# Kernel optimization log

Measured on AMD Instinct MI355X. Metric: run time of the kernel, lower is better.

Reference implementation:

```python
import jax, jax.numpy as jnp
import numpy as np

N_ATOM = 30000
N_PAIR = 1_000_000
N_TRI = 4_000_000
N_SF = 16
RC = 6.0

LAMBD = jnp.array([-1.0, 1.0] * 8, dtype=jnp.float32)
ZETA = jnp.array([1.0, 1.0, 2.0, 2.0, 4.0, 4.0, 8.0, 8.0] * 2, dtype=jnp.float32)
ETA = jnp.array([0.01, 0.014, 0.02, 0.028, 0.04, 0.056, 0.08, 0.11,
                 0.16, 0.22, 0.32, 0.45, 0.63, 0.72, 0.9, 1.0], dtype=jnp.float32)


def cutoff_f1(r):
    # PiNN 'f1' cutoff: 0.5*(cos(pi*r/rc)+1)
    return 0.5 * (jnp.cos(jnp.float32(np.pi) * r / RC) + 1.0)


def gaussian_basis(r, fc):
    # GaussianBasis with center=0, gamma=eta: fc * exp(-eta * r^2), shape [n, n_sf]
    return fc[:, None] * jnp.exp(-ETA[None, :] * (r[:, None] ** 2))


def setup_inputs() -> dict:
    key = jax.random.key(0)
    k1, k2, k3, k4, k5 = jax.random.split(key, 5)
    ind_2 = jax.random.randint(k1, (N_PAIR, 2), 0, N_ATOM, dtype=jnp.int32)
    ind_3 = jax.random.randint(k2, (N_TRI, 2), 0, N_PAIR, dtype=jnp.int32)
    dist = jax.random.uniform(k3, (N_PAIR,), jnp.float32, 0.5, RC)
    dirs = jax.random.normal(k4, (N_PAIR, 3), jnp.float32)
    dirs = dirs / jnp.linalg.norm(dirs, axis=1, keepdims=True)
    diff = dirs * dist[:, None]  # bond vectors consistent with dist
    elems = jax.random.randint(k5, (N_ATOM,), 0, 4, dtype=jnp.int32)
    fc = cutoff_f1(dist)
    return {"ind_2": ind_2, "ind_3": ind_3, "dist": dist, "diff": diff,
            "elems": elems, "fc": fc}


def reference(ind_2, ind_3, dist, diff, elems, fc):
    # i=j=k='ALL': species filter is identity; a_rind = arange(n_atom)
    ind_ij = ind_3[:, 0]
    ind_ik = ind_3[:, 1]
    i_rind = ind_2[ind_ij, 0]  # central atom index per triplet

    diff_ij = diff[ind_ij]  # [T,3]
    diff_ik = diff[ind_ik]
    diff_jk = diff_ik - diff_ij
    dist_jk = jnp.linalg.norm(diff_jk, axis=1)
    mask = dist_jk < RC  # TF filters triplets; we mask (jit-friendly)

    fc_jk = cutoff_f1(dist_jk)
    dist_ij = dist[ind_ij]
    dist_ik = dist[ind_ik]
    fc_ij = fc[ind_ij]
    fc_ik = fc[ind_ik]

    cos_ijk = jnp.einsum('id,id->i', diff_ij, diff_ik) / dist_ij / dist_ik
    base = jnp.maximum(1.0 + LAMBD[None, :] * cos_ijk[:, None], 0.0)
    sf = (2.0 ** (1.0 - ZETA[None, :]) * base ** ZETA[None, :]
          * gaussian_basis(dist_ij, fc_ij)
          * gaussian_basis(dist_ik, fc_ik)
          * gaussian_basis(dist_jk, fc_jk))
    sf = jnp.where(mask[:, None], sf, 0.0)

    # scatter_nd add into per-atom fingerprints
    fp = jnp.zeros((N_ATOM, N_SF), dtype=sf.dtype).at[i_rind].add(sf)

    # jacobian indices: central-atom rel index per participating pair
    vals = jnp.where(mask, i_rind, -1)
    seg = jnp.concatenate([ind_ij, ind_ik])
    pair_i = jax.ops.segment_max(jnp.concatenate([vals, vals]), seg,
                                 num_segments=N_PAIR)
    pair_i = jnp.maximum(pair_i, -1)  # empty segments -> -1 sentinel
    jacob_ind = jnp.stack([jnp.arange(N_PAIR, dtype=jnp.int32), pair_i], axis=1)
    return fp, jacob_ind
```

## Files before the change

kernel.cpp:

```cpp
#include <hip/hip_runtime.h>

#define N_ATOM 30000
#define N_PAIR 1000000
#define N_TRI  4000000
#define N_SF   16
#define FP_ELEMS (N_ATOM * N_SF)

#define ASH  5
#define APB  32
#define NCB  938
#define NSUB 8
#define NSEG (NCB * NSUB)
#define OVF_CNT_IDX NSEG
#define OVF_CAP 131072
#define TILE 4096
#define PER_TH 16
#define NTILES ((N_TRI + TILE - 1) / TILE)

#define OFF_CCNT  0ULL
#define OFF_IKMAX 65536ULL
#define OFF_AOFP  4065536ULL
#define OFF_FLAG  6065536ULL
#define OFF_OVF   7065536ULL
#define OFF_PACK  8114112ULL
#define OFF_CB    24114112ULL

__device__ __constant__ float c_eta[16] = {
    0.01f, 0.014f, 0.02f, 0.028f, 0.04f, 0.056f, 0.08f, 0.11f,
    0.16f, 0.22f, 0.32f, 0.45f, 0.63f, 0.72f, 0.9f, 1.0f};

__device__ __forceinline__ bool tri_math_pack(
    float4 A, float4 B, float A8[8], float& R2)
{
    float ax = A.x, ay = A.y, az = A.z, fcij = A.w;
    float bx = B.x, by = B.y, bz = B.z, fcik = B.w;
    float d2ij = fmaf(ax, ax, fmaf(ay, ay, az * az));
    float d2ik = fmaf(bx, bx, fmaf(by, by, bz * bz));
    float jx = bx - ax, jy = by - ay, jz = bz - az;
    float d2jk = fmaf(jx, jx, fmaf(jy, jy, jz * jz));
    if (!(d2jk < 36.0f)) return false;
    float dij = sqrtf(d2ij);
    float dik = sqrtf(d2ik);
    float djk = sqrtf(d2jk);
    const float PI_OVER_RC = 0.5235987755982988f;
    float fcjk = 0.5f * (__cosf(PI_OVER_RC * djk) + 1.0f);
    float dot = fmaf(ax, bx, fmaf(ay, by, az * bz));
    float cosv = dot / (dij * dik);
    R2 = d2ij + d2ik + d2jk;
    float FCt = fcij * fcik * fcjk;
    float bm = fmaxf(1.0f - cosv, 0.0f);
    float bp = fmaxf(1.0f + cosv, 0.0f);
    float bm2 = bm * bm, bp2 = bp * bp;
    float bm4 = bm2 * bm2, bp4 = bp2 * bp2;
    float bm8 = bm4 * bm4, bp8 = bp4 * bp4;
    A8[0] = FCt * bm;              A8[1] = FCt * bp;
    A8[2] = 0.5f * FCt * bm2;      A8[3] = 0.5f * FCt * bp2;
    A8[4] = 0.125f * FCt * bm4;    A8[5] = 0.125f * FCt * bp4;
    A8[6] = 0.0078125f * FCt * bm8; A8[7] = 0.0078125f * FCt * bp8;
    return true;
}


__global__ __launch_bounds__(256) void prep2(
    const int2* __restrict__ ind2, const float* __restrict__ diff,
    const float* __restrict__ fc,
    int* __restrict__ ccnt, int* __restrict__ ikmax,
    unsigned short* __restrict__ aofp, unsigned char* __restrict__ flag,
    float4* __restrict__ pack, float* __restrict__ out)
{
    int p = blockIdx.x * blockDim.x + threadIdx.x;
    if (p <= NSEG) ccnt[p] = 0;
    if (p < FP_ELEMS) out[p] = 0.0f;
    if (p >= N_PAIR) return;
    ikmax[p] = -1;
    flag[p] = 0;
    aofp[p] = (unsigned short)ind2[p].x;
    float4 r;
    r.x = diff[3 * p + 0];
    r.y = diff[3 * p + 1];
    r.z = diff[3 * p + 2];
    r.w = fc[p];
    pack[p] = r;
}

__global__ __launch_bounds__(256) void bin3(
    const int2* __restrict__ ind3, const unsigned short* __restrict__ aofp,
    int* __restrict__ ccnt, int2* __restrict__ cbucket,
    int2* __restrict__ ovf, int cap)
{
    __shared__ int lcnt[NCB];
    __shared__ int lbase[NCB];
    const int thr = threadIdx.x;
    const int sub = blockIdx.x & (NSUB - 1);
    const long long t0 = (long long)blockIdx.x * TILE;

    for (int i = thr; i < NCB; i += 256) lcnt[i] = 0;
    __syncthreads();

    int myatom[PER_TH];
    int myslot[PER_TH];
#pragma unroll
    for (int j = 0; j < PER_TH; ++j) {
        long long t = t0 + j * 256 + thr;
        int a = 0, s = -1;
        if (t < N_TRI) {
            int ij = ind3[t].x;
            a = aofp[ij];
            s = atomicAdd(&lcnt[a >> ASH], 1);
        }
        myatom[j] = a;
        myslot[j] = s;
    }
    __syncthreads();
    for (int c = thr; c < NCB; c += 256) {
        int n = lcnt[c];
        lbase[c] = n ? atomicAdd(&ccnt[c * NSUB + sub], n) : 0;
    }
    __syncthreads();
#pragma unroll
    for (int j = 0; j < PER_TH; ++j) {
        long long t = t0 + j * 256 + thr;
        if (t >= N_TRI) continue;
        int a = myatom[j];
        int c = a >> ASH;
        int slot = lbase[c] + myslot[j];
        int2 pr = ind3[t];
        if (slot < cap) {
            int2 e;
            e.x = pr.x | ((a & (APB - 1)) << 20);
            e.y = pr.y;
            cbucket[(size_t)(c * NSUB + sub) * cap + slot] = e;
        } else {
            int o = atomicAdd(&ccnt[OVF_CNT_IDX], 1);
            if (o < OVF_CAP) ovf[o] = pr;
        }
    }
}

__global__ __launch_bounds__(256) void reduce4(
    const int* __restrict__ ccnt, const int2* __restrict__ cbucket, int cap,
    const float4* __restrict__ pack,
    int* __restrict__ ikmax, unsigned char* __restrict__ flag,
    float* __restrict__ out)
{
    __shared__ float lacc[APB * 17];
    const int seg = blockIdx.x;
    const int b = seg >> 3;
    const int thr = threadIdx.x;
    for (int i = thr; i < APB * 17; i += 256) lacc[i] = 0.0f;
    __syncthreads();

    int n = ccnt[seg];
    n = min(n, cap);
    const int2* segp = cbucket + (size_t)seg * cap;
    for (int i = thr; i < n; i += 256) {
        int2 e = segp[i];
        int a5 = (e.x >> 20) & (APB - 1);
        int ij = e.x & 0xFFFFF;
        int ik = e.y;
        float4 A = pack[ij];
        float4 B = pack[ik];
        float A8[8], R2;
        if (!tri_math_pack(A, B, A8, R2)) continue;
        flag[ij] = 1;
        atomicMax(&ikmax[ik], (b << ASH) + a5);
#pragma unroll
        for (int s = 0; s < 16; ++s)
            atomicAdd(&lacc[a5 * 17 + s], A8[s & 7] * __expf(-c_eta[s] * R2));
    }
    __syncthreads();
    for (int t = thr; t < APB * N_SF; t += 256) {
        int atom = (b << ASH) + (t >> 4);
        float v = lacc[(t >> 4) * 17 + (t & 15)];
        if (atom < N_ATOM && v != 0.0f)
            unsafeAtomicAdd(out + (size_t)atom * N_SF + (t & 15), v);
    }
}

__global__ __launch_bounds__(256) void ovf3(
    const int* __restrict__ ccnt, const int2* __restrict__ ovf,
    const float4* __restrict__ pack, const unsigned short* __restrict__ aofp,
    int* __restrict__ ikmax, unsigned char* __restrict__ flag,
    float* __restrict__ out)
{
    int i = blockIdx.x * blockDim.x + threadIdx.x;
    int n = ccnt[OVF_CNT_IDX];
    if (n > OVF_CAP) n = OVF_CAP;
    if (i >= n) return;
    int2 pr = ovf[i];
    int ij = pr.x, ik = pr.y;
    float A8[8], R2;
    if (!tri_math_pack(pack[ij], pack[ik], A8, R2)) return;
    int atom = aofp[ij];
    flag[ij] = 1;
    atomicMax(&ikmax[ik], atom);
    float* base = out + (size_t)atom * N_SF;
#pragma unroll
    for (int s = 0; s < 16; ++s)
        unsafeAtomicAdd(base + s, A8[s & 7] * __expf(-c_eta[s] * R2));
}

__global__ __launch_bounds__(256) void fin3(
    const int* __restrict__ ikmax, const unsigned char* __restrict__ flag,
    const unsigned short* __restrict__ aofp, float* __restrict__ out)
{
    int p = blockIdx.x * blockDim.x + threadIdx.x;
    if (p >= N_PAIR) return;
    int v = ikmax[p];
    if (flag[p]) { int a = aofp[p]; v = v > a ? v : a; }
    float* jf = out + FP_ELEMS;
    jf[2 * p + 0] = (float)p;
    jf[2 * p + 1] = (float)v;
}


__global__ __launch_bounds__(256) void init_legacy(float* __restrict__ out) {
    int i = blockIdx.x * blockDim.x + threadIdx.x;
    if (i < FP_ELEMS) out[i] = 0.0f;
    if (i < N_PAIR) ((int*)out + FP_ELEMS)[2 * i + 1] = -1;
}

__global__ __launch_bounds__(256) void tri_legacy(
    const int* __restrict__ ind2, const int2* __restrict__ ind3,
    const float* __restrict__ dist, const float* __restrict__ diff,
    const float* __restrict__ fc, float* __restrict__ out) {
    int t = blockIdx.x * blockDim.x + threadIdx.x;
    if (t >= N_TRI) return;
    int2 pr = ind3[t];
    int ij = pr.x, ik = pr.y;
    float4 A, B;
    A.x = diff[3 * ij + 0]; A.y = diff[3 * ij + 1]; A.z = diff[3 * ij + 2]; A.w = fc[ij];
    B.x = diff[3 * ik + 0]; B.y = diff[3 * ik + 1]; B.z = diff[3 * ik + 2]; B.w = fc[ik];
    float A8[8], R2;
    if (!tri_math_pack(A, B, A8, R2)) return;
    int atom = ind2[2 * ij];
    int* jac = (int*)out + FP_ELEMS;
    atomicMax(&jac[2 * ij + 1], atom);
    atomicMax(&jac[2 * ik + 1], atom);
    float* base = out + (size_t)atom * N_SF;
#pragma unroll
    for (int s = 0; s < 16; ++s)
        unsafeAtomicAdd(base + s, A8[s & 7] * __expf(-c_eta[s] * R2));
}

__global__ __launch_bounds__(256) void fin_legacy(float* __restrict__ out) {
    int p = blockIdx.x * blockDim.x + threadIdx.x;
    if (p >= N_PAIR) return;
    int* jac = (int*)out + FP_ELEMS;
    int v = jac[2 * p + 1];
    float* jf = (float*)jac;
    jf[2 * p + 0] = (float)p;
    jf[2 * p + 1] = (float)v;
}


extern "C" void kernel_launch(void* const* d_in, const int* in_sizes, int n_in,
                              void* d_out, int out_size, void* d_ws, size_t ws_size,
                              hipStream_t stream) {
    const int2*  ind2 = (const int2*)d_in[0];
    const int2*  ind3 = (const int2*)d_in[1];
    const float* dist = (const float*)d_in[2];
    const float* diff = (const float*)d_in[3];
    const float* fc   = (const float*)d_in[5];
    float* out = (float*)d_out;

    const size_t seg_stride = (size_t)NSEG * sizeof(int2);
    const size_t need_min = OFF_CB + seg_stride * 608;

    if (ws_size >= need_min) {
        char* ws = (char*)d_ws;
        int* ccnt            = (int*)(ws + OFF_CCNT);
        int* ikmax           = (int*)(ws + OFF_IKMAX);
        unsigned short* aofp = (unsigned short*)(ws + OFF_AOFP);
        unsigned char* flag  = (unsigned char*)(ws + OFF_FLAG);
        int2* ovf            = (int2*)(ws + OFF_OVF);
        float4* pack         = (float4*)(ws + OFF_PACK);
        int2* cbucket        = (int2*)(ws + OFF_CB);
        int cap = (int)((ws_size - OFF_CB) / seg_stride);
        if (cap > 1024) cap = 1024;

        int pb = (N_PAIR + 255) / 256;
        prep2<<<pb, 256, 0, stream>>>(ind2, diff, fc, ccnt, ikmax, aofp, flag, pack, out);
        bin3<<<NTILES, 256, 0, stream>>>(ind3, aofp, ccnt, cbucket, ovf, cap);
        reduce4<<<NSEG, 256, 0, stream>>>(ccnt, cbucket, cap, pack, ikmax, flag, out);
        ovf3<<<OVF_CAP / 256, 256, 0, stream>>>(ccnt, ovf, pack, aofp, ikmax, flag, out);
        fin3<<<pb, 256, 0, stream>>>(ikmax, flag, aofp, out);
    } else {
        init_legacy<<<(N_PAIR + 255) / 256, 256, 0, stream>>>(out);
        tri_legacy<<<(N_PAIR * 4 + 255) / 256, 256, 0, stream>>>((const int*)d_in[0], ind3, dist, diff, fc, out);
        fin_legacy<<<(N_PAIR + 255) / 256, 256, 0, stream>>>(out);
    }
}
```

Before: 447.5 us.

## Rework binning tile size and reduce kernel to wave-per-segment with unrolled gathers

The binning kernel now uses 512-thread blocks over 8192-triplet tiles and packs each triplet's atom id and local slot into one register, cutting register use. The reduction kernel is restructured so that each 64-lane wave handles one sub-segment, two waves per block share a chunk's LDS accumulator, and bucket entries plus pair gathers are issued four at a time ahead of the math to expose more memory-level parallelism. Sharing LDS accumulators across two sub-segments halves the number of global flush atomics. The risk is higher register pressure from the unrolled gathers and fewer sub-buckets per bin, since larger tiles make each sub-bucket fill faster and push more triplets into the overflow path.

```diff
diff --git a/kernel.cpp b/kernel.cpp
--- a/kernel.cpp
+++ b/kernel.cpp
@@ -13,9 +13,10 @@
 #define NSEG (NCB * NSUB)
 #define OVF_CNT_IDX NSEG
 #define OVF_CAP 131072
-#define TILE 4096
+#define TILE 8192
 #define PER_TH 16
 #define NTILES ((N_TRI + TILE - 1) / TILE)
+#define RUNROLL 4
 
 #define OFF_CCNT  0ULL
 #define OFF_IKMAX 65536ULL
@@ -83,7 +84,7 @@
     pack[p] = r;
 }
 
-__global__ __launch_bounds__(256) void bin3(
+__global__ __launch_bounds__(512) void bin3(
     const int2* __restrict__ ind3, const unsigned short* __restrict__ aofp,
     int* __restrict__ ccnt, int2* __restrict__ cbucket,
     int2* __restrict__ ovf, int cap)
@@ -94,36 +95,36 @@
     const int sub = blockIdx.x & (NSUB - 1);
     const long long t0 = (long long)blockIdx.x * TILE;
 
-    for (int i = thr; i < NCB; i += 256) lcnt[i] = 0;
-    __syncthreads();
-
-    int myatom[PER_TH];
-    int myslot[PER_TH];
+    for (int i = thr; i < NCB; i += 512) lcnt[i] = 0;
+    __syncthreads();
+
+    unsigned mypack[PER_TH];
 #pragma unroll
     for (int j = 0; j < PER_TH; ++j) {
-        long long t = t0 + j * 256 + thr;
-        int a = 0, s = -1;
+        long long t = t0 + j * 512 + thr;
+        unsigned mp = 0;
         if (t < N_TRI) {
             int ij = ind3[t].x;
-            a = aofp[ij];
-            s = atomicAdd(&lcnt[a >> ASH], 1);
-        }
-        myatom[j] = a;
-        myslot[j] = s;
-    }
-    __syncthreads();
-    for (int c = thr; c < NCB; c += 256) {
+            int a = aofp[ij];
+            int s = atomicAdd(&lcnt[a >> ASH], 1);
+            mp = ((unsigned)s << 15) | (unsigned)a;
+        }
+        mypack[j] = mp;
+    }
+    __syncthreads();
+    for (int c = thr; c < NCB; c += 512) {
         int n = lcnt[c];
         lbase[c] = n ? atomicAdd(&ccnt[c * NSUB + sub], n) : 0;
     }
     __syncthreads();
 #pragma unroll
     for (int j = 0; j < PER_TH; ++j) {
-        long long t = t0 + j * 256 + thr;
+        long long t = t0 + j * 512 + thr;
         if (t >= N_TRI) continue;
-        int a = myatom[j];
+        unsigned mp = mypack[j];
+        int a = (int)(mp & 0x7FFF);
         int c = a >> ASH;
-        int slot = lbase[c] + myslot[j];
+        int slot = lbase[c] + (int)(mp >> 15);
         int2 pr = ind3[t];
         if (slot < cap) {
             int2 e;
@@ -137,39 +138,57 @@
     }
 }
 
-__global__ __launch_bounds__(256) void reduce4(
+__global__ __launch_bounds__(128) void reduce5(
     const int* __restrict__ ccnt, const int2* __restrict__ cbucket, int cap,
     const float4* __restrict__ pack,
     int* __restrict__ ikmax, unsigned char* __restrict__ flag,
     float* __restrict__ out)
 {
     __shared__ float lacc[APB * 17];
-    const int seg = blockIdx.x;
-    const int b = seg >> 3;
     const int thr = threadIdx.x;
-    for (int i = thr; i < APB * 17; i += 256) lacc[i] = 0.0f;
-    __syncthreads();
-
-    int n = ccnt[seg];
-    n = min(n, cap);
+    const int w = thr >> 6, lane = thr & 63;
+    const int b = blockIdx.x >> 2;
+    const int seg = (b << 3) + ((blockIdx.x & 3) << 1) + w;
+    for (int i = thr; i < APB * 17; i += 128) lacc[i] = 0.0f;
+    __syncthreads();
+
+    int n = min(ccnt[seg], cap);
     const int2* segp = cbucket + (size_t)seg * cap;
-    for (int i = thr; i < n; i += 256) {
-        int2 e = segp[i];
-        int a5 = (e.x >> 20) & (APB - 1);
-        int ij = e.x & 0xFFFFF;
-        int ik = e.y;
-        float4 A = pack[ij];
-        float4 B = pack[ik];
-        float A8[8], R2;
-        if (!tri_math_pack(A, B, A8, R2)) continue;
-        flag[ij] = 1;
-        atomicMax(&ikmax[ik], (b << ASH) + a5);
-#pragma unroll
-        for (int s = 0; s < 16; ++s)
-            atomicAdd(&lacc[a5 * 17 + s], A8[s & 7] * __expf(-c_eta[s] * R2));
-    }
-    __syncthreads();
-    for (int t = thr; t < APB * N_SF; t += 256) {
+
+    for (int base = 0; base < n; base += 64 * RUNROLL) {
+        int2 e[RUNROLL];
+        float4 A[RUNROLL], B[RUNROLL];
+        bool act[RUNROLL];
+#pragma unroll
+        for (int k = 0; k < RUNROLL; ++k) {
+            int idx = base + (k << 6) + lane;
+            act[k] = idx < n;
+            e[k] = segp[act[k] ? idx : 0];
+        }
+#pragma unroll
+        for (int k = 0; k < RUNROLL; ++k) {
+            int ij = e[k].x & 0xFFFFF;
+            int ik = e[k].y;
+            A[k] = pack[ij];
+            B[k] = pack[ik];
+        }
+#pragma unroll
+        for (int k = 0; k < RUNROLL; ++k) {
+            if (!act[k]) continue;
+            int a5 = (e[k].x >> 20) & (APB - 1);
+            int ij = e[k].x & 0xFFFFF;
+            int ik = e[k].y;
+            float A8[8], R2;
+            if (!tri_math_pack(A[k], B[k], A8, R2)) continue;
+            flag[ij] = 1;
+            atomicMax(&ikmax[ik], (b << ASH) + a5);
+#pragma unroll
+            for (int s = 0; s < 16; ++s)
+                atomicAdd(&lacc[a5 * 17 + s], A8[s & 7] * __expf(-c_eta[s] * R2));
+        }
+    }
+    __syncthreads();
+    for (int t = thr; t < APB * N_SF; t += 128) {
         int atom = (b << ASH) + (t >> 4);
         float v = lacc[(t >> 4) * 17 + (t & 15)];
         if (atom < N_ATOM && v != 0.0f)
@@ -281,13 +300,13 @@
 
         int pb = (N_PAIR + 255) / 256;
         prep2<<<pb, 256, 0, stream>>>(ind2, diff, fc, ccnt, ikmax, aofp, flag, pack, out);
-        bin3<<<NTILES, 256, 0, stream>>>(ind3, aofp, ccnt, cbucket, ovf, cap);
-        reduce4<<<NSEG, 256, 0, stream>>>(ccnt, cbucket, cap, pack, ikmax, flag, out);
+        bin3<<<NTILES, 512, 0, stream>>>(ind3, aofp, ccnt, cbucket, ovf, cap);
+        reduce5<<<NSEG / 2, 128, 0, stream>>>(ccnt, cbucket, cap, pack, ikmax, flag, out);
         ovf3<<<OVF_CAP / 256, 256, 0, stream>>>(ccnt, ovf, pack, aofp, ikmax, flag, out);
         fin3<<<pb, 256, 0, stream>>>(ikmax, flag, aofp, out);
     } else {
         init_legacy<<<(N_PAIR + 255) / 256, 256, 0, stream>>>(out);
-        tri_legacy<<<(N_PAIR * 4 + 255) / 256, 256, 0, stream>>>((const int*)d_in[0], ind3, dist, diff, fc, out);
+        tri_legacy<<<(N_TRI + 255) / 256, 256, 0, stream>>>((const int*)d_in[0], ind3, dist, diff, fc, out);
         fin_legacy<<<(N_PAIR + 255) / 256, 256, 0, stream>>>(out);
     }
 }
```

New measurement: 454.9 us. About the same (+1.7%).
